# Kernel tuning notes

Hardware: AMD Instinct MI355X
Metric: run time of the kernel (lower is better)

The kernel has to match this reference:

```python
import jax, jax.numpy as jnp
import numpy as np
import math

D, S, B = 64, 2048, 16  # head_dim, seq_len, batch (inputs stored as [D, S, B])


def setup_inputs() -> dict:
    key = jax.random.key(0)
    kq, kk, kv = jax.random.split(key, 3)
    return {
        "Q": jax.random.normal(kq, (D, S, B), dtype=jnp.float32),
        "K": jax.random.normal(kk, (D, S, B), dtype=jnp.float32),
        "V": jax.random.normal(kv, (D, S, B), dtype=jnp.float32),
        "d_k": S,
    }


def reference(Q, K, V, d_k):
    # transpose(0, 2): [D, S, B] -> [B, S, D]
    q = jnp.transpose(Q, (2, 1, 0))
    k = jnp.transpose(K, (2, 1, 0))
    v = jnp.transpose(V, (2, 1, 0))
    # bmm(_Q, K_T) * 1/sqrt(d_k): [B, S, S]
    scores = jnp.einsum("bsd,btd->bst", q, k) * (1.0 / math.sqrt(d_k))
    # original does view(-1, d_k) + Softmax over dim=1; with d_k == last dim
    # this is a softmax over the key axis. Dropout is identity in eval mode.
    probs = jax.nn.softmax(scores, axis=-1)
    out = jnp.einsum("bst,btd->bsd", probs, v)  # [B, S, D]
    # transpose(0, 2) back: [D, S, B]
    return jnp.transpose(out, (2, 1, 0))
```

## Files before the change

### kernel.cpp

```cpp
#include <hip/hip_runtime.h>

#define D_ 64
#define S_ 2048
#define B_ 16
#define QT 64
#define KVT 128

typedef short short8 __attribute__((ext_vector_type(8)));
typedef short short4a __attribute__((ext_vector_type(4)));
typedef float floatx4 __attribute__((ext_vector_type(4)));
typedef unsigned uint2v __attribute__((ext_vector_type(2)));

#define SC2 (1.4426950408889634f / 45.254833995939045f)

__device__ __forceinline__ unsigned short f2bf(float f) {
  unsigned u = __builtin_bit_cast(unsigned, f);
  u += 0x7fffu + ((u >> 16) & 1u);
  return (unsigned short)(u >> 16);
}

__device__ __forceinline__ floatx4 mfma16(short4a a, short4a b, floatx4 c) {
  return __builtin_amdgcn_mfma_f32_16x16x16bf16_1k(a, b, c, 0, 0, 0);
}

__global__ __launch_bounds__(256) void pack_all(const float* __restrict__ Q,
                                                const float* __restrict__ K,
                                                const float* __restrict__ V,
                                                unsigned short* __restrict__ Qp,
                                                unsigned short* __restrict__ Kp,
                                                unsigned short* __restrict__ Vt) {
  __shared__ __align__(16) unsigned short tile[256][72];
  const int t = threadIdx.x;
  const int bid = blockIdx.x;
  if (bid < 256) {
    const bool isK = bid >= 128;
    const float* src = isK ? K : Q;
    unsigned short* dst = isK ? Kp : Qp;
    const float scale = isK ? SC2 : 1.0f;
    const int s0 = (bid & 127) * 16;
#pragma unroll
    for (int i = 0; i < 16; i++) {
      int j = i * 256 + t;
      int d = j >> 6;
      int sb4 = (j & 63) * 4;
      const float4 v = *(const float4*)(src + (size_t)d * (S_ * B_) + s0 * B_ + sb4);
      float vv[4] = {v.x, v.y, v.z, v.w};
#pragma unroll
      for (int k = 0; k < 4; k++) {
        int sb = sb4 + k;
        int row = (sb & 15) * 16 + (sb >> 4);
        int sw = (((row >> 3) & 1) << 3) | (((row >> 6) & 3) << 4);
        tile[row][d ^ sw] = f2bf(vv[k] * scale);
      }
    }
    __syncthreads();
#pragma unroll
    for (int i = 0; i < 8; i++) {
      int j = i * 256 + t;
      int r = j >> 3, c = j & 7;
      int b = r >> 4, si = r & 15;
      int sw = (((r >> 3) & 1) << 3) | (((r >> 6) & 3) << 4);
      uint4 v = *(const uint4*)(&tile[r][(c * 8) ^ sw]);
      *(uint4*)(dst + ((size_t)(b * S_ + s0 + si) * D_ + c * 8)) = v;
    }
  } else {
    const int vb = bid - 256;
    const int s0 = (vb & 31) * 64;
    const int d0 = (vb >> 5) * 16;
#pragma unroll
    for (int i = 0; i < 16; i++) {
      int j = i * 256 + t;
      int dd = j >> 8;
      int sb4 = (j & 255) * 4;
      const float4 v = *(const float4*)(V + (size_t)(d0 + dd) * (S_ * B_) + s0 * B_ + sb4);
      float vv[4] = {v.x, v.y, v.z, v.w};
#pragma unroll
      for (int k = 0; k < 4; k++) {
        int sb = sb4 + k;
        int row = (sb & 15) * 16 + dd;
        int sw = ((row >> 6) & 3) << 3;
        tile[row][(sb >> 4) ^ sw] = f2bf(vv[k]);
      }
    }
    __syncthreads();
#pragma unroll
    for (int i = 0; i < 8; i++) {
      int j = i * 256 + t;
      int r = j >> 3, c = j & 7;
      int b = r >> 4, dd = r & 15;
      int sw = ((r >> 6) & 3) << 3;
      uint4 v = *(const uint4*)(&tile[r][(c * 8) ^ sw]);
      *(uint4*)(Vt + ((size_t)(b * D_ + d0 + dd) * S_ + s0 + c * 8)) = v;
    }
  }
}

__global__ __launch_bounds__(256, 2) void attn(const unsigned short* __restrict__ Qp,
                                               const unsigned short* __restrict__ Kp,
                                               const unsigned short* __restrict__ Vt,
                                               float* __restrict__ Ot) {
  __shared__ __align__(16) char smem_[71680 + 1024];
  float* red = (float*)smem_;
  float* lred = (float*)(smem_ + 71680);

  const int tid = threadIdx.x;
  const int w = tid >> 6, l = tid & 63, g = l >> 4, ln = l & 15;
  const int b = blockIdx.x & 15;
  const int q0 = (int)(blockIdx.x >> 4) * QT;
  const int kvw = w * 32;

  const unsigned short* Qb = Qp + (size_t)b * S_ * D_;
  const unsigned short* Kb = Kp + (size_t)b * S_ * D_;
  const unsigned short* Vb = Vt + (size_t)b * D_ * S_;

  const int rk = tid >> 3, ck = tid & 7;
  const int rv = tid >> 4, cv = tid & 15;

  {
    unsigned short* Ks0 = (unsigned short*)(smem_);
    unsigned short* Vs0 = (unsigned short*)(smem_ + 18432);
#pragma unroll
    for (int i = 0; i < 4; i++) {
      uint4 kv4 = *(const uint4*)(Kb + (size_t)(i * 32 + rk) * D_ + ck * 8);
      *(uint4*)(&Ks0[(i * 32 + rk) * 72 + ck * 8]) = kv4;
      uint4 vv4 = *(const uint4*)(Vb + (size_t)(i * 16 + rv) * S_ + cv * 8);
      *(uint4*)(&Vs0[(i * 16 + rv) * 136 + cv * 8]) = vv4;
    }
  }

  short8 qf[4][2];
#pragma unroll
  for (int nf = 0; nf < 4; nf++)
#pragma unroll
    for (int ks = 0; ks < 2; ks++)
      qf[nf][ks] = *(const short8*)(Qb + (size_t)(q0 + nf * 16 + ln) * D_ + ks * 32 + g * 8);

  floatx4 oacc[4][4];
#pragma unroll
  for (int mfd = 0; mfd < 4; mfd++)
#pragma unroll
    for (int nf = 0; nf < 4; nf++) oacc[mfd][nf] = (floatx4){0.f, 0.f, 0.f, 0.f};
  float lpart[4] = {0.f, 0.f, 0.f, 0.f};

  __syncthreads();

  for (int t = 0; t < 16; t++) {
    const int cur = t & 1, nxt = cur ^ 1;
    const int kvn = ((t + 1) * KVT) & (S_ - 1);
    unsigned short* Ksc = (unsigned short*)(smem_ + cur * 35840);
    unsigned short* Vsc = (unsigned short*)(smem_ + 18432 + cur * 35840);

    uint4 kstg[4], vstg[4];
    if (t < 15) {
#pragma unroll
      for (int i = 0; i < 4; i++) {
        kstg[i] = *(const uint4*)(Kb + (size_t)(kvn + i * 32 + rk) * D_ + ck * 8);
        vstg[i] = *(const uint4*)(Vb + (size_t)(i * 16 + rv) * S_ + kvn + cv * 8);
      }
    }

    short8 kf[2][2];
#pragma unroll
    for (int mf = 0; mf < 2; mf++)
#pragma unroll
      for (int ks = 0; ks < 2; ks++)
        kf[mf][ks] = *(const short8*)(&Ksc[(kvw + mf * 16 + ln) * 72 + ks * 32 + g * 8]);
    floatx4 sacc[2][4];
#pragma unroll
    for (int mf = 0; mf < 2; mf++)
#pragma unroll
      for (int nf = 0; nf < 4; nf++) sacc[mf][nf] = (floatx4){0.f, 0.f, 0.f, 0.f};
#pragma unroll
    for (int ks = 0; ks < 2; ks++)
#pragma unroll
      for (int mf = 0; mf < 2; mf++)
#pragma unroll
        for (int nf = 0; nf < 4; nf++)
          sacc[mf][nf] = __builtin_amdgcn_mfma_f32_16x16x32_bf16(kf[mf][ks], qf[nf][ks],
                                                                 sacc[mf][nf], 0, 0, 0);

    short4a pb[2][4];
#pragma unroll
    for (int mf = 0; mf < 2; mf++)
#pragma unroll
      for (int nf = 0; nf < 4; nf++) {
        float p0 = __builtin_amdgcn_exp2f(sacc[mf][nf][0]);
        float p1 = __builtin_amdgcn_exp2f(sacc[mf][nf][1]);
        float p2 = __builtin_amdgcn_exp2f(sacc[mf][nf][2]);
        float p3 = __builtin_amdgcn_exp2f(sacc[mf][nf][3]);
        lpart[nf] += (p0 + p1) + (p2 + p3);
        unsigned u0 = __builtin_bit_cast(unsigned, p0) + 0x8000u;
        unsigned u1 = __builtin_bit_cast(unsigned, p1) + 0x8000u;
        unsigned u2 = __builtin_bit_cast(unsigned, p2) + 0x8000u;
        unsigned u3 = __builtin_bit_cast(unsigned, p3) + 0x8000u;
        unsigned lo = __builtin_amdgcn_perm(u1, u0, 0x07060302u);
        unsigned hi = __builtin_amdgcn_perm(u3, u2, 0x07060302u);
        pb[mf][nf] = __builtin_bit_cast(short4a, (uint2v){lo, hi});
      }

#pragma unroll
    for (int mfd = 0; mfd < 4; mfd++)
#pragma unroll
      for (int mf = 0; mf < 2; mf++) {
        short4a vf = *(const short4a*)(&Vsc[(mfd * 16 + ln) * 136 + kvw + mf * 16 + g * 4]);
#pragma unroll
        for (int nf = 0; nf < 4; nf++)
          oacc[mfd][nf] = mfma16(vf, pb[mf][nf], oacc[mfd][nf]);
      }

    if (t < 15) {
      unsigned short* Ksn = (unsigned short*)(smem_ + nxt * 35840);
      unsigned short* Vsn = (unsigned short*)(smem_ + 18432 + nxt * 35840);
#pragma unroll
      for (int i = 0; i < 4; i++) {
        *(uint4*)(&Ksn[(i * 32 + rk) * 72 + ck * 8]) = kstg[i];
        *(uint4*)(&Vsn[(i * 16 + rv) * 136 + cv * 8]) = vstg[i];
      }
      __syncthreads();
    }
  }

  float lsum[4];
#pragma unroll
  for (int nf = 0; nf < 4; nf++) {
    float v = lpart[nf];
    v += __shfl_xor(v, 16);
    v += __shfl_xor(v, 32);
    lsum[nf] = v;
  }
  __syncthreads();
  if (g == 0) {
#pragma unroll
    for (int nf = 0; nf < 4; nf++) lred[w * 64 + nf * 16 + ln] = lsum[nf];
  }
#pragma unroll
  for (int mfd = 0; mfd < 4; mfd++)
#pragma unroll
    for (int nf = 0; nf < 4; nf++)
      *(floatx4*)(&red[w * 4352 + (nf * 16 + ln) * 68 + mfd * 16 + g * 4]) = oacc[mfd][nf];
  __syncthreads();

  const int q = l;
  const float denom = lred[q] + lred[64 + q] + lred[128 + q] + lred[192 + q];
  const float linv = 1.0f / denom;
#pragma unroll
  for (int i = 0; i < 4; i++) {
    floatx4 s = (floatx4){0.f, 0.f, 0.f, 0.f};
#pragma unroll
    for (int w2 = 0; w2 < 4; w2++)
      s += *(const floatx4*)(&red[w2 * 4352 + q * 68 + w * 16 + i * 4]);
    s *= linv;
#pragma unroll
    for (int r = 0; r < 4; r++)
      Ot[(size_t)(b * D_ + w * 16 + i * 4 + r) * S_ + q0 + q] = s[r];
  }
}

__global__ __launch_bounds__(256) void unpack_o(const float* __restrict__ Ot,
                                                float* __restrict__ out) {
  const int d0 = (int)(blockIdx.x & 7) * 8;
  const int s0 = (int)(blockIdx.x >> 3) * 64;
  __shared__ float u[8 * 1024];
  const int t = threadIdx.x;
#pragma unroll
  for (int i = 0; i < 8; i++) {
    int j = i * 256 + t;
    int d = j >> 8, bb = (j >> 4) & 15, c = j & 15;
    float4 v = *(const float4*)(Ot + (size_t)(bb * D_ + d0 + d) * S_ + s0 + c * 4);
    float vv[4] = {v.x, v.y, v.z, v.w};
#pragma unroll
    for (int k = 0; k < 4; k++) {
      int si = c * 4 + k;
      int W = si * 16 + bb;
      int Wp = W ^ ((si & 15) << 2);
      u[d * 1024 + Wp] = vv[k];
    }
  }
  __syncthreads();
#pragma unroll
  for (int i = 0; i < 8; i++) {
    int j = i * 256 + t;
    int d = j >> 8, c2 = j & 255;
    int G = c2 ^ ((c2 >> 2) & 15);
    float4 v = *(const float4*)(&u[d * 1024 + G * 4]);
    *(float4*)(out + (size_t)(d0 + d) * (S_ * B_) + s0 * B_ + c2 * 4) = v;
  }
}

extern "C" void kernel_launch(void* const* d_in, const int* in_sizes, int n_in,
                              void* d_out, int out_size, void* d_ws, size_t ws_size,
                              hipStream_t stream) {
  const float* Q = (const float*)d_in[0];
  const float* K = (const float*)d_in[1];
  const float* V = (const float*)d_in[2];
  float* out = (float*)d_out;
  char* ws = (char*)d_ws;
  unsigned short* Qp = (unsigned short*)(ws);
  unsigned short* Kp = (unsigned short*)(ws + (4u << 20));
  unsigned short* Vt = (unsigned short*)(ws + (8u << 20));
  float* Ot = (float*)(ws + (12u << 20));

  hipLaunchKernelGGL(pack_all, dim3(384), dim3(256), 0, stream, Q, K, V, Qp, Kp, Vt);
  hipLaunchKernelGGL(attn, dim3(512), dim3(256), 0, stream, Qp, Kp, Vt, Ot);
  hipLaunchKernelGGL(unpack_o, dim3(256), dim3(256), 0, stream, Ot, out);
}
```

Baseline: 110.9 us.

## Split KV sequence across two blocks and merge partial outputs in unpack

The attention kernel now splits the key/value sequence into two halves, launching twice as many blocks, each writing unnormalized partial outputs and denominators to workspace. The unpack kernel sums the two partials, divides by the combined denominator, and transposes. Shared memory drops to a single K/V buffer with an extra barrier and a two-pass epilogue, allowing four blocks per CU in place of two. This trades the loss of double-buffered loads and extra partial-output traffic for more blocks in flight on the GPU.

```diff
diff --git a/kernel.cpp b/kernel.cpp
--- a/kernel.cpp
+++ b/kernel.cpp
@@ -95,18 +95,21 @@
   }
 }
 
-__global__ __launch_bounds__(256, 2) void attn(const unsigned short* __restrict__ Qp,
+__global__ __launch_bounds__(256, 4) void attn(const unsigned short* __restrict__ Qp,
                                                const unsigned short* __restrict__ Kp,
                                                const unsigned short* __restrict__ Vt,
-                                               float* __restrict__ Ot) {
-  __shared__ __align__(16) char smem_[71680 + 1024];
+                                               float* __restrict__ Otp,
+                                               float* __restrict__ Dp) {
+  __shared__ __align__(16) char smem_[36864 + 1024];
   float* red = (float*)smem_;
-  float* lred = (float*)(smem_ + 71680);
+  float* lred = (float*)(smem_ + 36864);
 
   const int tid = threadIdx.x;
   const int w = tid >> 6, l = tid & 63, g = l >> 4, ln = l & 15;
   const int b = blockIdx.x & 15;
-  const int q0 = (int)(blockIdx.x >> 4) * QT;
+  const int q0 = (int)((blockIdx.x >> 4) & 31) * QT;
+  const int kvh = (int)(blockIdx.x >> 9);
+  const int kvb = kvh << 10;
   const int kvw = w * 32;
 
   const unsigned short* Qb = Qp + (size_t)b * S_ * D_;
@@ -117,14 +120,14 @@
   const int rv = tid >> 4, cv = tid & 15;
 
   {
-    unsigned short* Ks0 = (unsigned short*)(smem_);
-    unsigned short* Vs0 = (unsigned short*)(smem_ + 18432);
+    unsigned short* Ks = (unsigned short*)smem_;
+    unsigned short* Vs = (unsigned short*)(smem_ + 18432);
 #pragma unroll
     for (int i = 0; i < 4; i++) {
-      uint4 kv4 = *(const uint4*)(Kb + (size_t)(i * 32 + rk) * D_ + ck * 8);
-      *(uint4*)(&Ks0[(i * 32 + rk) * 72 + ck * 8]) = kv4;
-      uint4 vv4 = *(const uint4*)(Vb + (size_t)(i * 16 + rv) * S_ + cv * 8);
-      *(uint4*)(&Vs0[(i * 16 + rv) * 136 + cv * 8]) = vv4;
+      uint4 kv4 = *(const uint4*)(Kb + (size_t)(kvb + i * 32 + rk) * D_ + ck * 8);
+      *(uint4*)(&Ks[(i * 32 + rk) * 72 + ck * 8]) = kv4;
+      uint4 vv4 = *(const uint4*)(Vb + (size_t)(i * 16 + rv) * S_ + kvb + cv * 8);
+      *(uint4*)(&Vs[(i * 16 + rv) * 136 + cv * 8]) = vv4;
     }
   }
 
@@ -144,14 +147,13 @@
 
   __syncthreads();
 
-  for (int t = 0; t < 16; t++) {
-    const int cur = t & 1, nxt = cur ^ 1;
-    const int kvn = ((t + 1) * KVT) & (S_ - 1);
-    unsigned short* Ksc = (unsigned short*)(smem_ + cur * 35840);
-    unsigned short* Vsc = (unsigned short*)(smem_ + 18432 + cur * 35840);
+  for (int t = 0; t < 8; t++) {
+    unsigned short* Ks = (unsigned short*)smem_;
+    unsigned short* Vs = (unsigned short*)(smem_ + 18432);
+    const int kvn = kvb + (t + 1) * KVT;
 
     uint4 kstg[4], vstg[4];
-    if (t < 15) {
+    if (t < 7) {
 #pragma unroll
       for (int i = 0; i < 4; i++) {
         kstg[i] = *(const uint4*)(Kb + (size_t)(kvn + i * 32 + rk) * D_ + ck * 8);
@@ -164,7 +166,7 @@
     for (int mf = 0; mf < 2; mf++)
 #pragma unroll
       for (int ks = 0; ks < 2; ks++)
-        kf[mf][ks] = *(const short8*)(&Ksc[(kvw + mf * 16 + ln) * 72 + ks * 32 + g * 8]);
+        kf[mf][ks] = *(const short8*)(&Ks[(kvw + mf * 16 + ln) * 72 + ks * 32 + g * 8]);
     floatx4 sacc[2][4];
 #pragma unroll
     for (int mf = 0; mf < 2; mf++)
@@ -202,19 +204,18 @@
     for (int mfd = 0; mfd < 4; mfd++)
 #pragma unroll
       for (int mf = 0; mf < 2; mf++) {
-        short4a vf = *(const short4a*)(&Vsc[(mfd * 16 + ln) * 136 + kvw + mf * 16 + g * 4]);
+        short4a vf = *(const short4a*)(&Vs[(mfd * 16 + ln) * 136 + kvw + mf * 16 + g * 4]);
 #pragma unroll
         for (int nf = 0; nf < 4; nf++)
           oacc[mfd][nf] = mfma16(vf, pb[mf][nf], oacc[mfd][nf]);
       }
 
-    if (t < 15) {
-      unsigned short* Ksn = (unsigned short*)(smem_ + nxt * 35840);
-      unsigned short* Vsn = (unsigned short*)(smem_ + 18432 + nxt * 35840);
+    __syncthreads();
+    if (t < 7) {
 #pragma unroll
       for (int i = 0; i < 4; i++) {
-        *(uint4*)(&Ksn[(i * 32 + rk) * 72 + ck * 8]) = kstg[i];
-        *(uint4*)(&Vsn[(i * 16 + rv) * 136 + cv * 8]) = vstg[i];
+        *(uint4*)(&Ks[(i * 32 + rk) * 72 + ck * 8]) = kstg[i];
+        *(uint4*)(&Vs[(i * 16 + rv) * 136 + cv * 8]) = vstg[i];
       }
       __syncthreads();
     }
@@ -228,52 +229,86 @@
     v += __shfl_xor(v, 32);
     lsum[nf] = v;
   }
-  __syncthreads();
   if (g == 0) {
 #pragma unroll
     for (int nf = 0; nf < 4; nf++) lred[w * 64 + nf * 16 + ln] = lsum[nf];
   }
-#pragma unroll
-  for (int mfd = 0; mfd < 4; mfd++)
+  const size_t oofs = (size_t)kvh * (B_ * D_ * S_);
+
+#pragma unroll
+  for (int mfd = 0; mfd < 2; mfd++)
 #pragma unroll
     for (int nf = 0; nf < 4; nf++)
-      *(floatx4*)(&red[w * 4352 + (nf * 16 + ln) * 68 + mfd * 16 + g * 4]) = oacc[mfd][nf];
-  __syncthreads();
-
+      *(floatx4*)(&red[w * 2304 + (nf * 16 + ln) * 36 + mfd * 16 + g * 4]) = oacc[mfd][nf];
+  __syncthreads();
   const int q = l;
   const float denom = lred[q] + lred[64 + q] + lred[128 + q] + lred[192 + q];
-  const float linv = 1.0f / denom;
-#pragma unroll
-  for (int i = 0; i < 4; i++) {
+  if (w == 0) Dp[(size_t)kvh * (B_ * S_) + b * S_ + q0 + q] = denom;
+#pragma unroll
+  for (int i = 0; i < 2; i++) {
     floatx4 s = (floatx4){0.f, 0.f, 0.f, 0.f};
 #pragma unroll
     for (int w2 = 0; w2 < 4; w2++)
-      s += *(const floatx4*)(&red[w2 * 4352 + q * 68 + w * 16 + i * 4]);
-    s *= linv;
+      s += *(const floatx4*)(&red[w2 * 2304 + q * 36 + w * 8 + i * 4]);
+    const int d = w * 8 + i * 4;
 #pragma unroll
     for (int r = 0; r < 4; r++)
-      Ot[(size_t)(b * D_ + w * 16 + i * 4 + r) * S_ + q0 + q] = s[r];
-  }
-}
-
-__global__ __launch_bounds__(256) void unpack_o(const float* __restrict__ Ot,
+      Otp[oofs + (size_t)(b * D_ + d + r) * S_ + q0 + q] = s[r];
+  }
+  __syncthreads();
+
+#pragma unroll
+  for (int mfd = 2; mfd < 4; mfd++)
+#pragma unroll
+    for (int nf = 0; nf < 4; nf++)
+      *(floatx4*)(&red[w * 2304 + (nf * 16 + ln) * 36 + (mfd - 2) * 16 + g * 4]) = oacc[mfd][nf];
+  __syncthreads();
+#pragma unroll
+  for (int i = 0; i < 2; i++) {
+    floatx4 s = (floatx4){0.f, 0.f, 0.f, 0.f};
+#pragma unroll
+    for (int w2 = 0; w2 < 4; w2++)
+      s += *(const floatx4*)(&red[w2 * 2304 + q * 36 + w * 8 + i * 4]);
+    const int d = 32 + w * 8 + i * 4;
+#pragma unroll
+    for (int r = 0; r < 4; r++)
+      Otp[oofs + (size_t)(b * D_ + d + r) * S_ + q0 + q] = s[r];
+  }
+}
+
+__global__ __launch_bounds__(256) void unpack_o(const float* __restrict__ Otp,
+                                                const float* __restrict__ Dp,
                                                 float* __restrict__ out) {
   const int d0 = (int)(blockIdx.x & 7) * 8;
   const int s0 = (int)(blockIdx.x >> 3) * 64;
   __shared__ float u[8 * 1024];
+  __shared__ float dinv[16 * 64];
   const int t = threadIdx.x;
+  {
+    int bb = t >> 4, si4 = (t & 15) * 4;
+    float4 a = *(const float4*)(Dp + bb * S_ + s0 + si4);
+    float4 c = *(const float4*)(Dp + (B_ * S_) + bb * S_ + s0 + si4);
+    dinv[bb * 64 + si4 + 0] = 1.0f / (a.x + c.x);
+    dinv[bb * 64 + si4 + 1] = 1.0f / (a.y + c.y);
+    dinv[bb * 64 + si4 + 2] = 1.0f / (a.z + c.z);
+    dinv[bb * 64 + si4 + 3] = 1.0f / (a.w + c.w);
+  }
+  __syncthreads();
 #pragma unroll
   for (int i = 0; i < 8; i++) {
     int j = i * 256 + t;
     int d = j >> 8, bb = (j >> 4) & 15, c = j & 15;
-    float4 v = *(const float4*)(Ot + (size_t)(bb * D_ + d0 + d) * S_ + s0 + c * 4);
-    float vv[4] = {v.x, v.y, v.z, v.w};
+    const float* p0 = Otp + (size_t)(bb * D_ + d0 + d) * S_ + s0 + c * 4;
+    float4 v0 = *(const float4*)p0;
+    float4 v1 = *(const float4*)(p0 + (size_t)B_ * D_ * S_);
+    float vv[4] = {v0.x + v1.x, v0.y + v1.y, v0.z + v1.z, v0.w + v1.w};
 #pragma unroll
     for (int k = 0; k < 4; k++) {
       int si = c * 4 + k;
+      float val = vv[k] * dinv[bb * 64 + si];
       int W = si * 16 + bb;
       int Wp = W ^ ((si & 15) << 2);
-      u[d * 1024 + Wp] = vv[k];
+      u[d * 1024 + Wp] = val;
     }
   }
   __syncthreads();
@@ -298,9 +333,10 @@
   unsigned short* Qp = (unsigned short*)(ws);
   unsigned short* Kp = (unsigned short*)(ws + (4u << 20));
   unsigned short* Vt = (unsigned short*)(ws + (8u << 20));
-  float* Ot = (float*)(ws + (12u << 20));
+  float* Otp = (float*)(ws + (12u << 20));
+  float* Dp  = (float*)(ws + (28u << 20));
 
   hipLaunchKernelGGL(pack_all, dim3(384), dim3(256), 0, stream, Q, K, V, Qp, Kp, Vt);
-  hipLaunchKernelGGL(attn, dim3(512), dim3(256), 0, stream, Qp, Kp, Vt, Ot);
-  hipLaunchKernelGGL(unpack_o, dim3(256), dim3(256), 0, stream, Ot, out);
-}
+  hipLaunchKernelGGL(attn, dim3(1024), dim3(256), 0, stream, Qp, Kp, Vt, Otp, Dp);
+  hipLaunchKernelGGL(unpack_o, dim3(256), dim3(256), 0, stream, Otp, Dp, out);
+}
```

New measurement: 218.1 us. 96.7% more time.
